# Kernel optimization log

Measured on AMD Instinct MI355X. Metric: run time of the kernel, lower is better.

Reference implementation:

```python
import jax, jax.numpy as jnp
import numpy as np

N = 100000          # nodes
E = 600000          # edges
H = 128             # hidden_dim
CF_DIM = 15         # input_dim - 1
NOISE_DIM = 32
NUM_CLASS = 6       # GraphConstructor.number_of_class
B = 64              # number of graphs in batch
BC = B * NUM_CLASS  # total clusters
LAYER_NUM = 3
NEG_SLOPE = 0.01


def setup_inputs() -> dict:
    key = jax.random.key(0)
    ks = jax.random.split(key, 12)
    cf = jax.random.normal(ks[0], (N, CF_DIM), jnp.float32)
    slf = jax.random.uniform(ks[1], (N,), jnp.float32)
    z = jax.random.normal(ks[2], (N, NOISE_DIM), jnp.float32)
    tr = jax.random.uniform(ks[3], (BC,), jnp.float32)
    W_enc = jax.random.normal(ks[4], (CF_DIM + 1 + NOISE_DIM, H), jnp.float32) * 0.05
    b_enc = jax.random.normal(ks[5], (H,), jnp.float32) * 0.05
    W_m = jax.random.normal(ks[6], (2 * H, H), jnp.float32) * 0.05
    b_m = jax.random.normal(ks[7], (H,), jnp.float32) * 0.05
    W_u = jax.random.normal(ks[8], (3 * H, H), jnp.float32) * 0.05
    b_u = jax.random.normal(ks[9], (H,), jnp.float32) * 0.05
    e = jax.random.randint(ks[10], (2, E), 0, N, jnp.int64)
    cc = jax.random.randint(ks[11], (N,), 0, BC, jnp.int64)
    cfb = cc // NUM_CLASS  # batch index consistent with global cluster index
    return {"cf": cf, "slf": slf, "z": z, "tr": tr,
            "W_enc": W_enc, "b_enc": b_enc, "W_m": W_m, "b_m": b_m,
            "W_u": W_u, "b_u": b_u, "e": e, "cc": cc, "cfb": cfb}


def _segment_mean(x, idx, num_segments):
    s = jax.ops.segment_sum(x, idx, num_segments=num_segments)
    c = jax.ops.segment_sum(jnp.ones((x.shape[0],), x.dtype), idx, num_segments=num_segments)
    return s / jnp.maximum(c, 1.0)[:, None]


def reference(cf, slf, z, tr, W_enc, b_enc, W_m, b_m, W_u, b_u, e, cc, cfb):
    # encoder: x = enc(cat(cf, slf, z))  (Linear, no activation since act='')
    x = jnp.concatenate([cf, slf[:, None], z], axis=-1) @ W_enc + b_enc  # [N, H]
    src, dst = e[0], e[1]  # PyG: x_j = x[src], x_i = x[dst], aggregate at dst
    for _ in range(LAYER_NUM):
        # message: MLP(cat(feature_i, feature_j)) per edge, mean-aggregated at dst
        msg = jnp.concatenate([x[dst], x[src]], axis=-1) @ W_m + b_m  # [E, H]
        aggr = _segment_mean(msg, dst, N)                              # [N, H]
        # cluster avg_pool scaled by target ratio, broadcast back to nodes
        pooled = _segment_mean(x, cc, BC) * tr[:, None]                # [BC, H]
        node_pool = pooled[cc]                                         # [N, H]
        upd = jnp.concatenate([x, aggr, node_pool], axis=-1) @ W_u + b_u
        upd = jnp.where(upd > 0, upd, NEG_SLOPE * upd)                 # LeakyReLU
        x = x + upd                                                    # residual
    return x
```

## Files before the change

### kernel.cpp

```cpp
#include <hip/hip_runtime.h>
#include <hip/hip_bf16.h>

#define N_NODES 100000
#define N_EDGES 600000
#define HD 128
#define NBC 384
#define SCAN_B 98
#define MAXFIX 4096
#define TILES ((N_NODES + 63) / 64)
#define GRID_F 521
#define AGG_B (N_NODES / 4)
#define CAPB 16384

typedef __attribute__((ext_vector_type(8))) short s8v;
typedef __attribute__((ext_vector_type(4))) short s4v;
typedef __attribute__((ext_vector_type(4))) float f4v;
typedef __hip_bfloat16 bf16;

static __device__ __forceinline__ float bf2f(bf16 v) { return __bfloat162float(v); }
static __device__ __forceinline__ bf16 f2bf(float v) { return __float2bfloat16(v); }
static __device__ __forceinline__ float sh2f(short s) { bf16 h = *(bf16*)&s; return bf2f(h); }
static __device__ __forceinline__ short f2sh(float v) { bf16 h = f2bf(v); return *(short*)&h; }
static __device__ __forceinline__ float ldraw(const void* p, int i, int fp32) {
    return fp32 ? ((const float*)p)[i] : bf2f(((const bf16*)p)[i]);
}

static __device__ __forceinline__ void gl2lds16(const void* g, void* l) {
    __builtin_amdgcn_global_load_lds(
        (const __attribute__((address_space(1))) void*)g,
        (__attribute__((address_space(3))) void*)l, 16, 0, 0);
}

__global__ void k_init(const unsigned short* __restrict__ wraw, const int* __restrict__ eraw,
                       int* __restrict__ flags, int* __restrict__ deg,
                       int* __restrict__ ccount, int* __restrict__ n0cnt,
                       int* __restrict__ bcur) {
    int b = blockIdx.x, t = threadIdx.x;
    if (b == 0) {
        if (t < 64) {
            int bad = 0;
            for (int k = 0; k < 16; k++) {
                unsigned int u = ((unsigned int)wraw[t * 16 + k]) << 16;
                float f = fabsf(__uint_as_float(u));
                if (!(f <= 1e4f)) bad = 1;
            }
            unsigned long long m = __ballot(bad);
            if (t == 0) {
                flags[0] = m ? 1 : 0;
                flags[1] = (eraw[1] == 0 && eraw[3] == 0 && eraw[5] == 0 && eraw[7] == 0) ? 1 : 0;
            }
        }
    } else if (b <= 98) {
        int i = (b - 1) * 256 + t;
        if (i < 25000) ((int4*)deg)[i] = make_int4(0, 0, 0, 0);
    } else {
        if (t < 96) ((int4*)ccount)[t] = make_int4(0, 0, 0, 0);
        if (t == 96) *n0cnt = 0;
        if (t >= 128 && t < 128 + SCAN_B) bcur[t - 128] = 0;
    }
}

#define F_EDGE 586
#define F_XIN  (F_EDGE + 391)
#define F_CC   (F_XIN + 391)
#define F_WU   (F_CC + 192)
#define F_WM   (F_WU + 128)
#define F_WET  (F_WM + 32)
#define F_BC   (F_WET + 1)
#define F_TR   (F_BC + 2)
__global__ void k_ffront(const int* __restrict__ flags,
                         const void* cf_r, const void* slf_r, const void* z_r,
                         const void* tr_r, const void* Wenc_r, const void* benc_r,
                         const void* Wm_r, const void* bm_r, const void* Wu_r,
                         const void* bu_r, const int* __restrict__ e_r,
                         const int* __restrict__ cc_r,
                         bf16* __restrict__ xin, bf16* __restrict__ trc,
                         bf16* __restrict__ Wuc, bf16* __restrict__ Wmc,
                         bf16* __restrict__ buc, int* __restrict__ ccc,
                         int* __restrict__ deg, int* __restrict__ ccount,
                         bf16* __restrict__ Wet, float* __restrict__ bc,
                         float* __restrict__ bcenc,
                         int* __restrict__ bcur, int* __restrict__ ebuf) {
    __shared__ short scfs[3840];
    __shared__ int hist[SCAN_B], hbase[SCAN_B], lcur[SCAN_B];
    int b = blockIdx.x, t = threadIdx.x;
    int fp32 = flags[0];
    if (b < F_EDGE) {
        int i64f = flags[1];
        int e0 = b * 1024;
        if (t < SCAN_B) { hist[t] = 0; lcur[t] = 0; }
        __syncthreads();
        int sv[4], dv[4], bk[4];
#pragma unroll
        for (int k = 0; k < 4; k++) {
            int i = e0 + k * 256 + t;
            if (i < N_EDGES) {
                sv[k] = i64f ? e_r[2 * i] : e_r[i];
                dv[k] = i64f ? e_r[2 * (N_EDGES + i)] : e_r[N_EDGES + i];
                bk[k] = dv[k] >> 10;
                atomicAdd(&hist[bk[k]], 1);
                atomicAdd(&deg[dv[k]], 1);
            } else bk[k] = -1;
        }
        __syncthreads();
        if (t < SCAN_B && hist[t] > 0) hbase[t] = atomicAdd(&bcur[t], hist[t]);
        __syncthreads();
#pragma unroll
        for (int k = 0; k < 4; k++) {
            if (bk[k] >= 0) {
                int rel = hbase[bk[k]] + atomicAdd(&lcur[bk[k]], 1);
                if (rel < CAPB) ebuf[bk[k] * CAPB + rel] = (sv[k] << 10) | (dv[k] & 1023);
            }
        }
    } else if (b < F_XIN) {
        int bb = b - F_EDGE;
        int base = bb * 256;
        int cnt = min(3840, 1500000 - base * 15);
        if (fp32) {
            const float* cfp = (const float*)cf_r + (size_t)base * 15;
            f4v c0, c1, c2, c3;
            int e0 = t * 4, e1 = (256 + t) * 4, e2 = (512 + t) * 4, e3 = (768 + t) * 4;
            if (e0 < cnt) c0 = *(const f4v*)(cfp + e0);
            if (e1 < cnt) c1 = *(const f4v*)(cfp + e1);
            if (e2 < cnt) c2 = *(const f4v*)(cfp + e2);
            if (e3 < cnt) c3 = *(const f4v*)(cfp + e3);
            if (e0 < cnt) { for (int j = 0; j < 4; j++) scfs[e0 + j] = f2sh(c0[j]); }
            if (e1 < cnt) { for (int j = 0; j < 4; j++) scfs[e1 + j] = f2sh(c1[j]); }
            if (e2 < cnt) { for (int j = 0; j < 4; j++) scfs[e2 + j] = f2sh(c2[j]); }
            if (e3 < cnt) { for (int j = 0; j < 4; j++) scfs[e3 + j] = f2sh(c3[j]); }
        } else {
            const short* cfp = (const short*)cf_r + (size_t)base * 15;
            s8v c0, c1;
            int e0 = t * 8, e1 = (256 + t) * 8;
            if (e0 < cnt) c0 = *(const s8v*)(cfp + e0);
            if (e1 < cnt) c1 = *(const s8v*)(cfp + e1);
            if (e0 < cnt) *(s8v*)(scfs + e0) = c0;
            if (e1 < cnt) *(s8v*)(scfs + e1) = c1;
        }
        __syncthreads();
        int node = base + t;
        if (node >= N_NODES) return;
        short* xr = (short*)xin + (size_t)node * 64;
        const short* c = scfs + t * 15;
        s8v o0, o1;
#pragma unroll
        for (int r = 0; r < 8; r++) o0[r] = c[r];
#pragma unroll
        for (int r = 0; r < 7; r++) o1[r] = c[8 + r];
        o1[7] = fp32 ? f2sh(((const float*)slf_r)[node]) : ((const short*)slf_r)[node];
        if (fp32) {
            const float* zp = (const float*)z_r + (size_t)node * 32;
            f4v z0 = *(const f4v*)(zp +  0), z1 = *(const f4v*)(zp +  4);
            f4v z2 = *(const f4v*)(zp +  8), z3 = *(const f4v*)(zp + 12);
            f4v z4 = *(const f4v*)(zp + 16), z5 = *(const f4v*)(zp + 20);
            f4v z6 = *(const f4v*)(zp + 24), z7 = *(const f4v*)(zp + 28);
            s8v w0, w1, w2, w3;
#pragma unroll
            for (int r = 0; r < 4; r++) {
                w0[r] = f2sh(z0[r]); w0[4 + r] = f2sh(z1[r]);
                w1[r] = f2sh(z2[r]); w1[4 + r] = f2sh(z3[r]);
                w2[r] = f2sh(z4[r]); w2[4 + r] = f2sh(z5[r]);
                w3[r] = f2sh(z6[r]); w3[4 + r] = f2sh(z7[r]);
            }
            *(s8v*)(xr) = o0; *(s8v*)(xr + 8) = o1;
            *(s8v*)(xr + 16) = w0; *(s8v*)(xr + 24) = w1;
            *(s8v*)(xr + 32) = w2; *(s8v*)(xr + 40) = w3;
        } else {
            const short* zp = (const short*)z_r + (size_t)node * 32;
            s8v w0 = *(const s8v*)(zp), w1 = *(const s8v*)(zp + 8);
            s8v w2 = *(const s8v*)(zp + 16), w3 = *(const s8v*)(zp + 24);
            *(s8v*)(xr) = o0; *(s8v*)(xr + 8) = o1;
            *(s8v*)(xr + 16) = w0; *(s8v*)(xr + 24) = w1;
            *(s8v*)(xr + 32) = w2; *(s8v*)(xr + 40) = w3;
        }
        s8v zz = {0, 0, 0, 0, 0, 0, 0, 0};
        *(s8v*)(xr + 48) = zz;
        *(s8v*)(xr + 56) = zz;
    } else if (b < F_CC) {
        int i64f = flags[1];
        int i = (b - F_XIN) * 256 + t;
        if (i < N_NODES) {
            int v = i64f ? cc_r[2 * i] : cc_r[i];
            ccc[i] = v;
            atomicAdd(&ccount[v], 1);
        }
    } else if (b < F_WU) {
        int i = (b - F_CC) * 256 + t;
        Wuc[i] = f2bf(ldraw(Wu_r, i, fp32));
    } else if (b < F_WM) {
        int i = (b - F_WU) * 256 + t;
        Wmc[i] = f2bf(ldraw(Wm_r, i, fp32));
    } else if (b < F_WET) {
        int i = (b - F_WM) * 256 + t;
        int w = i >> 6, kk = i & 63;
        float v = (kk < 48) ? ldraw(Wenc_r, kk * 128 + w, fp32) : 0.f;
        Wet[i] = f2bf(v);
    } else if (b < F_BC) {
        if (t < 128) {
            float acc = ldraw(bu_r, t, fp32);
            for (int j = 0; j < 128; j++)
                acc += ldraw(bm_r, j, fp32) * ldraw(Wu_r, (128 + j) * 128 + t, fp32);
            bc[t] = acc;
        } else {
            bcenc[t - 128] = ldraw(benc_r, t - 128, fp32);
            buc[t - 128] = f2bf(ldraw(bu_r, t - 128, fp32));
        }
    } else {
        int i = (b - F_BC) * 256 + t;
        if (i < 384) trc[i] = f2bf(ldraw(tr_r, i, fp32));
    }
}

__global__ void k_scan_a2(const int* __restrict__ deg, int* __restrict__ rowptr,
                          int* __restrict__ bsum, const int* __restrict__ ccount,
                          int* __restrict__ coff, int* __restrict__ ccur) {
    __shared__ int sd[1024];
    int t = threadIdx.x;
    if (blockIdx.x < SCAN_B) {
        int i = blockIdx.x * 1024 + t;
        int v = (i < N_NODES) ? deg[i] : 0;
        sd[t] = v;
        __syncthreads();
#pragma unroll
        for (int off = 1; off < 1024; off <<= 1) {
            int u = (t >= off) ? sd[t - off] : 0;
            __syncthreads();
            sd[t] += u;
            __syncthreads();
        }
        if (i < N_NODES) rowptr[i] = sd[t] - v;
        if (t == 1023) bsum[blockIdx.x] = sd[t];
    } else {
        int v = (t < NBC) ? ccount[t] : 0;
        sd[t] = v;
        __syncthreads();
#pragma unroll
        for (int off = 1; off < 1024; off <<= 1) {
            int u = (t >= off) ? sd[t - off] : 0;
            __syncthreads();
            sd[t] += u;
            __syncthreads();
        }
        if (t < NBC) {
            int ex = sd[t] - v;
            coff[t] = ex;
            ccur[t] = ex;
            if (t == NBC - 1) coff[NBC] = sd[t];
        }
    }
}

#define M_SC 98
#define M_W  (M_SC + 6)
#define M_CF (M_W + 98)
#define M_L0 (M_CF + 98)
__global__ void k_mid(int* __restrict__ rowptr, const int* __restrict__ bsum,
                      const bf16* __restrict__ Wmc, const bf16* __restrict__ Wuc,
                      bf16* __restrict__ Wc,
                      const int* __restrict__ ccc, int* __restrict__ ccur,
                      int* __restrict__ cnodes,
                      const int* __restrict__ deg, int* __restrict__ n0list,
                      int* __restrict__ n0cnt) {
    __shared__ short wm[4][2048];
    __shared__ int h[NBC], cb[NBC];
    __shared__ int sb[128];
    __shared__ int offs;
    int b = blockIdx.x, t = threadIdx.x;
    if (b < M_SC) {
        if (t < 128) sb[t] = (t < b) ? bsum[t] : 0;
        __syncthreads();
        if (t == 0) {
            int s = 0;
            for (int k = 0; k < 128; k++) s += sb[k];
            offs = s;
        }
        __syncthreads();
        int i = b * 1024 + t;
        if (i < N_NODES) rowptr[i] = rowptr[i] + offs;
        if (b == 0 && t == 0) rowptr[N_NODES] = N_EDGES;
    } else if (b < M_W) {
        int kw = b - M_SC;
        int sub = t >> 8, lt = t & 255;
        int bp = kw * 4 + sub;
        int w = lt & 127, g = lt >> 7;
        int kk0 = bp * 16 + g * 8;
        if (kk0 >= 256) {
            s8v ov;
#pragma unroll
            for (int n = 0; n < 8; n++)
                ov[n] = *((const short*)Wuc + (kk0 + n) * 128 + w);
            *(s8v*)((short*)Wc + w * 384 + kk0) = ov;
            return;
        }
        *(s8v*)(wm[sub] + lt * 8) = *(const s8v*)((const short*)Wmc + bp * 2048 + lt * 8);
        __syncthreads();
        float acc[8];
#pragma unroll
        for (int n = 0; n < 8; n++) acc[n] = 0.f;
        const short* wup = (const short*)Wuc + 128 * 128 + w;
        const short* wmb = wm[sub] + (g * 8) * 128;
#pragma unroll 4
        for (int j = 0; j < 128; j++) {
            float wu = sh2f(wup[j * 128]);
#pragma unroll
            for (int n = 0; n < 8; n++)
                acc[n] += sh2f(wmb[n * 128 + j]) * wu;
        }
        s8v ov;
#pragma unroll
        for (int n = 0; n < 8; n++) {
            int kk = kk0 + n;
            float base = (kk < 128) ? sh2f(*((const short*)Wuc + kk * 128 + w)) : 0.f;
            ov[n] = f2sh(acc[n] + base);
        }
        *(s8v*)((short*)Wc + w * 384 + kk0) = ov;
    } else if (b < M_CF) {
        int base = (b - M_W) << 10;
        int node = base + t;
        if (t < NBC) h[t] = 0;
        __syncthreads();
        int cls = (node < N_NODES) ? ccc[node] : -1;
        if (cls >= 0) atomicAdd(&h[cls], 1);
        __syncthreads();
        if (t < NBC) {
            cb[t] = h[t] ? atomicAdd(&ccur[t], h[t]) : 0;
            h[t] = 0;
        }
        __syncthreads();
        if (cls >= 0) {
            int p = cb[cls] + atomicAdd(&h[cls], 1);
            cnodes[p] = node;
        }
    } else {
        int i = (b - M_CF) * 1024 + t;
        if (i < N_NODES && deg[i] == 0) {
            int p = atomicAdd(n0cnt, 1);
            if (p < MAXFIX) n0list[p] = i;
        }
    }
}

#define K5_EN 1563
#define K5_PC (K5_EN + SCAN_B)
__global__ void k_front(const bf16* __restrict__ xin, const bf16* __restrict__ Wet,
                        const float* __restrict__ bcenc, bf16* __restrict__ xb,
                        const int* __restrict__ rowptr, const int* __restrict__ ebuf,
                        int* __restrict__ colx) {
    __shared__ int cur[1024];
    int b = blockIdx.x;
    if (b >= K5_EN) {
        int bb = b - K5_EN;
        int base = bb << 10;
        int nlim = min(1024, N_NODES - base);
        for (int i = threadIdx.x; i < nlim; i += 256) cur[i] = rowptr[base + i];
        __syncthreads();
        int cnt = rowptr[base + nlim] - rowptr[base];
        const int* eb = ebuf + bb * CAPB;
        for (int e = threadIdx.x; e < cnt; e += 256) {
            int v = eb[e];
            int p = atomicAdd(&cur[v & 1023], 1);
            colx[p] = v >> 10;
        }
        return;
    }
    int tid = threadIdx.x;
    int r0 = b * 64;
    int wave = tid >> 6, lane = tid & 63, quad = lane >> 4, nidx = lane & 15;
    int colbase = wave * 32;

    int arow[4];
#pragma unroll
    for (int rt = 0; rt < 4; rt++) {
        int gr = r0 + rt * 16 + nidx;
        arow[rt] = (gr < N_NODES) ? gr : (N_NODES - 1);
    }
    f4v acc[4][2];
#pragma unroll
    for (int rt = 0; rt < 4; rt++)
#pragma unroll
        for (int ct = 0; ct < 2; ct++) acc[rt][ct] = (f4v){0.f, 0.f, 0.f, 0.f};

#pragma unroll
    for (int s = 0; s < 2; s++) {
        int k0 = s * 32;
        s8v bfrag[4];
#pragma unroll
        for (int rt = 0; rt < 4; rt++)
            bfrag[rt] = *(const s8v*)((const short*)xin + (size_t)arow[rt] * 64 + k0 + quad * 8);
#pragma unroll
        for (int ct = 0; ct < 2; ct++) {
            s8v wfr = *(const s8v*)((const short*)Wet + (colbase + ct * 16 + nidx) * 64 + k0 + quad * 8);
#pragma unroll
            for (int rt = 0; rt < 4; rt++)
                acc[rt][ct] = __builtin_amdgcn_mfma_f32_16x16x32_bf16(wfr, bfrag[rt], acc[rt][ct], 0, 0, 0);
        }
    }
#pragma unroll
    for (int rt = 0; rt < 4; rt++) {
        int gr = r0 + rt * 16 + nidx;
        if (gr < N_NODES) {
#pragma unroll
            for (int ct = 0; ct < 2; ct++) {
                int wc0 = colbase + ct * 16 + quad * 4;
                f4v bv = *(const f4v*)(bcenc + wc0);
                size_t idx = (size_t)gr * HD + wc0;
                s4v ob;
#pragma unroll
                for (int r = 0; r < 4; r++) ob[r] = f2sh(acc[rt][ct][r] + bv[r]);
                *(s4v*)((short*)xb + idx) = ob;
            }
        }
    }
}

__global__ void k_aggpool(const bf16* __restrict__ xb, const int* __restrict__ rowptr,
                          const int* __restrict__ colx, bf16* __restrict__ mb,
                          const int* __restrict__ coff, const int* __restrict__ cnodes,
                          const bf16* __restrict__ trc, bf16* __restrict__ pooled) {
    __shared__ float red[8][128];
    int tid = threadIdx.x;
    if (blockIdx.x < NBC) {
        int cl = blockIdx.x;
        int lo = coff[cl], hi = coff[cl + 1];
        int cnt = hi - lo;
        int slot = tid >> 5, cg = tid & 31;
        float a0 = 0.f, a1 = 0.f, a2 = 0.f, a3 = 0.f;
        for (int i = lo + slot; i < hi; i += 8) {
            int nd = cnodes[i];
            s4v v = *(const s4v*)((const short*)xb + (size_t)nd * HD + cg * 4);
            a0 += sh2f(v[0]); a1 += sh2f(v[1]); a2 += sh2f(v[2]); a3 += sh2f(v[3]);
        }
        red[slot][cg * 4 + 0] = a0;
        red[slot][cg * 4 + 1] = a1;
        red[slot][cg * 4 + 2] = a2;
        red[slot][cg * 4 + 3] = a3;
        __syncthreads();
        if (tid < 128) {
            float s = 0.f;
#pragma unroll
            for (int k = 0; k < 8; k++) s += red[k][tid];
            float v = s / (float)(cnt > 1 ? cnt : 1) * bf2f(trc[cl]);
            pooled[cl * HD + tid] = f2bf(v);
        }
        return;
    }
    int wave = tid >> 6, lane = tid & 63;
    int node = (blockIdx.x - NBC) * 4 + wave;
    if (node >= N_NODES) return;
    int half = lane >> 5;
    int l = lane & 31;
    int lo = rowptr[node], hi = rowptr[node + 1];
    float a0 = 0.f, a1 = 0.f, a2 = 0.f, a3 = 0.f;
    for (int j0 = lo + half; j0 < hi; j0 += 8) {
        int i1 = j0 + 2, i2 = j0 + 4, i3 = j0 + 6;
        int s0 = colx[j0];
        int s1 = colx[i1 < hi ? i1 : j0];
        int s2 = colx[i2 < hi ? i2 : j0];
        int s3 = colx[i3 < hi ? i3 : j0];
        float m1 = (i1 < hi) ? 1.f : 0.f;
        float m2 = (i2 < hi) ? 1.f : 0.f;
        float m3 = (i3 < hi) ? 1.f : 0.f;
        s4v v0 = *(const s4v*)((const short*)xb + (size_t)s0 * HD + l * 4);
        s4v v1 = *(const s4v*)((const short*)xb + (size_t)s1 * HD + l * 4);
        s4v v2 = *(const s4v*)((const short*)xb + (size_t)s2 * HD + l * 4);
        s4v v3 = *(const s4v*)((const short*)xb + (size_t)s3 * HD + l * 4);
        a0 += sh2f(v0[0]) + m1 * sh2f(v1[0]) + m2 * sh2f(v2[0]) + m3 * sh2f(v3[0]);
        a1 += sh2f(v0[1]) + m1 * sh2f(v1[1]) + m2 * sh2f(v2[1]) + m3 * sh2f(v3[1]);
        a2 += sh2f(v0[2]) + m1 * sh2f(v1[2]) + m2 * sh2f(v2[2]) + m3 * sh2f(v3[2]);
        a3 += sh2f(v0[3]) + m1 * sh2f(v1[3]) + m2 * sh2f(v2[3]) + m3 * sh2f(v3[3]);
    }
    a0 += __shfl_down(a0, 32);
    a1 += __shfl_down(a1, 32);
    a2 += __shfl_down(a2, 32);
    a3 += __shfl_down(a3, 32);
    if (half == 0) {
        int d = hi - lo;
        float inv = 1.0f / (float)(d > 1 ? d : 1);
        s4v o;
        o[0] = f2sh(a0 * inv); o[1] = f2sh(a1 * inv);
        o[2] = f2sh(a2 * inv); o[3] = f2sh(a3 * inv);
        *(s4v*)((short*)mb + (size_t)node * HD + l * 4) = o;
    }
}

__global__ __launch_bounds__(256, 2) void k_fused2(
    const bf16* __restrict__ xb, const bf16* __restrict__ mb, const bf16* __restrict__ pooled,
    const bf16* __restrict__ Wc, const float* __restrict__ bc,
    const int* __restrict__ cc, const int* __restrict__ deg,
    const bf16* __restrict__ Wuc, const bf16* __restrict__ buc,
    const int* __restrict__ n0list, const int* __restrict__ n0cnt,
    bf16* __restrict__ xbo, const int* __restrict__ flags,
    void* __restrict__ out, int last) {
    __shared__ short Lx[64 * 128];
    __shared__ short Lm[64 * 128];
    __shared__ short Lp[64 * 128];
    __shared__ float fxv[128];
    __shared__ float fpv[128];
    int tid = threadIdx.x;
    int wave = tid >> 6, lane = tid & 63, quad = lane >> 4, nidx = lane & 15;
    int colbase = wave * 32;
    int fp32out = flags[0];

    s8v wfr[12][2];
#pragma unroll
    for (int ct = 0; ct < 2; ct++) {
        int wcol = colbase + ((nidx >> 2) << 3) + ct * 4 + (nidx & 3);
        const short* wrow = (const short*)Wc + (size_t)wcol * 384 + quad * 8;
#pragma unroll
        for (int s = 0; s < 12; s++) wfr[s][ct] = *(const s8v*)(wrow + s * 32);
    }
    int cb2 = colbase + quad * 8;
    f4v bv0 = *(const f4v*)(bc + cb2);
    f4v bv1 = *(const f4v*)(bc + cb2 + 4);

    int srow = lane >> 4;
    int sc = lane & 15;

    for (int t = blockIdx.x; t < TILES; t += GRID_F) {
        int r0 = t * 64;
#pragma unroll
        for (int ii = 0; ii < 4; ii++) {
            int i = wave * 4 + ii;
            int lr = i * 4 + srow;
            int gr = r0 + lr;
            int grc = (gr < N_NODES) ? gr : (N_NODES - 1);
            int gc = sc ^ (lr & 15);
            gl2lds16((const short*)xb + (size_t)grc * HD + gc * 8, (char*)Lx + i * 1024);
            gl2lds16((const short*)mb + (size_t)grc * HD + gc * 8, (char*)Lm + i * 1024);
            int ci = cc[grc];
            gl2lds16((const short*)pooled + (size_t)ci * HD + gc * 8, (char*)Lp + i * 1024);
        }
        __syncthreads();

        f4v acc[4][2];
#pragma unroll
        for (int rt = 0; rt < 4; rt++)
#pragma unroll
            for (int ct = 0; ct < 2; ct++) acc[rt][ct] = (f4v){0.f, 0.f, 0.f, 0.f};

#pragma unroll
        for (int s = 0; s < 12; s++) {
            const short* Ls = (s < 4) ? Lx : ((s < 8) ? Lm : Lp);
            int c = (s & 3) * 4 + quad;
            s8v bfrag[4];
#pragma unroll
            for (int rt = 0; rt < 4; rt++) {
                int row = rt * 16 + nidx;
                int slot = c ^ nidx;
                bfrag[rt] = *(const s8v*)(Ls + row * 128 + slot * 8);
            }
#pragma unroll
            for (int ct = 0; ct < 2; ct++)
#pragma unroll
                for (int rt = 0; rt < 4; rt++)
                    acc[rt][ct] = __builtin_amdgcn_mfma_f32_16x16x32_bf16(wfr[s][ct], bfrag[rt], acc[rt][ct], 0, 0, 0);
        }

#pragma unroll
        for (int rt = 0; rt < 4; rt++) {
            int gr = r0 + rt * 16 + nidx;
            if (gr < N_NODES && deg[gr] > 0) {
                int row = rt * 16 + nidx;
                int slot = ((colbase >> 3) + quad) ^ nidx;
                s8v xo = *(const s8v*)(Lx + row * 128 + slot * 8);
                size_t idx = (size_t)gr * HD + cb2;
                float nv[8];
#pragma unroll
                for (int r = 0; r < 4; r++) {
                    float v0 = acc[rt][0][r] + bv0[r];
                    v0 = (v0 > 0.f) ? v0 : 0.01f * v0;
                    nv[r] = sh2f(xo[r]) + v0;
                    float v1 = acc[rt][1][r] + bv1[r];
                    v1 = (v1 > 0.f) ? v1 : 0.01f * v1;
                    nv[4 + r] = sh2f(xo[4 + r]) + v1;
                }
                if (last) {
                    if (fp32out) {
                        f4v o0 = {nv[0], nv[1], nv[2], nv[3]};
                        f4v o1 = {nv[4], nv[5], nv[6], nv[7]};
                        *(f4v*)((float*)out + idx) = o0;
                        *(f4v*)((float*)out + idx + 4) = o1;
                    } else {
                        s8v ob;
#pragma unroll
                        for (int r = 0; r < 8; r++) ob[r] = f2sh(nv[r]);
                        *(s8v*)((short*)out + idx) = ob;
                    }
                } else {
                    s8v ob;
#pragma unroll
                    for (int r = 0; r < 8; r++) ob[r] = f2sh(nv[r]);
                    *(s8v*)((short*)xbo + idx) = ob;
                }
            }
        }
        __syncthreads();
    }

    int cnt0 = *n0cnt;
    if (cnt0 > MAXFIX) cnt0 = MAXFIX;
    for (int j = blockIdx.x; j < cnt0; j += gridDim.x) {
        int v = n0list[j];
        if (tid < 128) {
            fxv[tid] = bf2f(xb[(size_t)v * HD + tid]);
            fpv[tid] = bf2f(pooled[cc[v] * HD + tid]);
        }
        __syncthreads();
        if (tid < 128) {
            float acc = bf2f(buc[tid]);
            for (int k = 0; k < 128; k++)
                acc += fxv[k] * bf2f(Wuc[k * 128 + tid]) + fpv[k] * bf2f(Wuc[(256 + k) * 128 + tid]);
            float u = acc > 0.f ? acc : 0.01f * acc;
            size_t idx = (size_t)v * HD + tid;
            float nv = fxv[tid] + u;
            if (last) {
                if (fp32out) ((float*)out)[idx] = nv;
                else ((bf16*)out)[idx] = f2bf(nv);
            } else {
                xbo[idx] = f2bf(nv);
            }
        }
        __syncthreads();
    }
}

extern "C" void kernel_launch(void* const* d_in, const int* in_sizes, int n_in,
                              void* d_out, int out_size, void* d_ws, size_t ws_size,
                              hipStream_t stream) {
    const void* cf_r = d_in[0];
    const void* slf_r = d_in[1];
    const void* z_r = d_in[2];
    const void* tr_r = d_in[3];
    const void* Wenc_r = d_in[4];
    const void* benc_r = d_in[5];
    const void* Wm_r = d_in[6];
    const void* bm_r = d_in[7];
    const void* Wu_r = d_in[8];
    const void* bu_r = d_in[9];
    const int* e_r = (const int*)d_in[10];
    const int* cc_r = (const int*)d_in[11];

    char* w = (char*)d_ws;
    auto alloc = [&](size_t bytes) -> char* {
        char* p = w;
        w += (bytes + 63) & ~(size_t)63;
        return p;
    };
    bf16* xb0 = (bf16*)alloc((size_t)N_NODES * HD * 2);
    bf16* xb1 = (bf16*)alloc((size_t)N_NODES * HD * 2);
    bf16* mb = (bf16*)alloc((size_t)N_NODES * HD * 2);
    bf16* xin = (bf16*)alloc((size_t)N_NODES * 64 * 2);
    bf16* Wc = (bf16*)alloc(128 * 384 * 2);
    float* bc = (float*)alloc(128 * 4);
    bf16* Wet = (bf16*)alloc(128 * 64 * 2);
    float* bcenc = (float*)alloc(128 * 4);
    bf16* pooled = (bf16*)alloc(NBC * HD * 2);
    int* deg = (int*)alloc(N_NODES * 4);
    int* rowptr = (int*)alloc((N_NODES + 1) * 4);
    int* colx = (int*)alloc(N_EDGES * 4);
    int* ccount = (int*)alloc(NBC * 4);
    int* coff = (int*)alloc((NBC + 1) * 4);
    int* ccur = (int*)alloc(NBC * 4);
    int* cnodes = (int*)alloc(N_NODES * 4);
    int* flags = (int*)alloc(64);
    int* bsum = (int*)alloc(SCAN_B * 4);
    int* n0list = (int*)alloc(MAXFIX * 4);
    int* n0cnt = (int*)alloc(64);
    bf16* trc = (bf16*)alloc(384 * 2);
    bf16* Wuc = (bf16*)alloc(49152 * 2);
    bf16* Wmc = (bf16*)alloc(32768 * 2);
    bf16* buc = (bf16*)alloc(128 * 2);
    int* ccc = (int*)alloc(N_NODES * 4);
    int* bcur = (int*)alloc(SCAN_B * 4);
    int* ebuf = (int*)alloc((size_t)SCAN_B * CAPB * 4);

    k_init<<<100, 256, 0, stream>>>((const unsigned short*)Wenc_r, e_r, flags,
                                    deg, ccount, n0cnt, bcur);
    k_ffront<<<F_TR, 256, 0, stream>>>(flags, cf_r, slf_r, z_r, tr_r, Wenc_r, benc_r,
                                       Wm_r, bm_r, Wu_r, bu_r, e_r, cc_r,
                                       xin, trc, Wuc, Wmc, buc, ccc, deg, ccount,
                                       Wet, bc, bcenc, bcur, ebuf);
    k_scan_a2<<<SCAN_B + 1, 1024, 0, stream>>>(deg, rowptr, bsum, ccount, coff, ccur);
    k_mid<<<M_L0, 1024, 0, stream>>>(rowptr, bsum, Wmc, Wuc, Wc,
                                     ccc, ccur, cnodes, deg, n0list, n0cnt);
    k_front<<<K5_PC, 256, 0, stream>>>(xin, Wet, bcenc, xb0, rowptr, ebuf, colx);

    bf16* xbufs[2] = {xb0, xb1};
    for (int layer = 0; layer < 3; layer++) {
        bf16* xbi = xbufs[layer & 1];
        bf16* xbo = xbufs[(layer + 1) & 1];
        int last = (layer == 2);
        k_aggpool<<<AGG_B + NBC, 256, 0, stream>>>(xbi, rowptr, colx, mb,
                                                   coff, cnodes, trc, pooled);
        k_fused2<<<GRID_F, 256, 0, stream>>>(xbi, mb, pooled, Wc, bc, ccc, deg,
                                             Wuc, buc, n0list, n0cnt,
                                             xbo, flags, d_out, last);
    }
}
```

Baseline: 446.1 us.

## Build CSR from destination buckets instead of global degree atomics and scan

The CSR build no longer uses per-edge global degree atomics and a 100K-element two-pass scan. Per-bucket degree histograms are now computed in LDS inside k_mid, with a small scan over bucket totals, and rowptr, deg, the zero-degree list and colx are all filled in that same block. Cluster counting now uses a per-block LDS histogram before the global atomics, and the old deg-zeroing blocks in k_init are removed. Together these cut global atomics and kernel work in the preprocessing phase. The cost is that each bucket is now handled by a single 1024-thread block doing serial LDS atomics.

```diff
diff --git a/kernel.cpp b/kernel.cpp
--- a/kernel.cpp
+++ b/kernel.cpp
@@ -32,9 +32,8 @@
 }
 
 __global__ void k_init(const unsigned short* __restrict__ wraw, const int* __restrict__ eraw,
-                       int* __restrict__ flags, int* __restrict__ deg,
-                       int* __restrict__ ccount, int* __restrict__ n0cnt,
-                       int* __restrict__ bcur) {
+                       int* __restrict__ flags, int* __restrict__ ccount,
+                       int* __restrict__ n0cnt, int* __restrict__ bcur) {
     int b = blockIdx.x, t = threadIdx.x;
     if (b == 0) {
         if (t < 64) {
@@ -50,9 +49,6 @@
                 flags[1] = (eraw[1] == 0 && eraw[3] == 0 && eraw[5] == 0 && eraw[7] == 0) ? 1 : 0;
             }
         }
-    } else if (b <= 98) {
-        int i = (b - 1) * 256 + t;
-        if (i < 25000) ((int4*)deg)[i] = make_int4(0, 0, 0, 0);
     } else {
         if (t < 96) ((int4*)ccount)[t] = make_int4(0, 0, 0, 0);
         if (t == 96) *n0cnt = 0;
@@ -62,7 +58,7 @@
 
 #define F_EDGE 586
 #define F_XIN  (F_EDGE + 391)
-#define F_CC   (F_XIN + 391)
+#define F_CC   (F_XIN + 98)
 #define F_WU   (F_CC + 192)
 #define F_WM   (F_WU + 128)
 #define F_WET  (F_WM + 32)
@@ -77,12 +73,13 @@
                          bf16* __restrict__ xin, bf16* __restrict__ trc,
                          bf16* __restrict__ Wuc, bf16* __restrict__ Wmc,
                          bf16* __restrict__ buc, int* __restrict__ ccc,
-                         int* __restrict__ deg, int* __restrict__ ccount,
+                         int* __restrict__ ccount,
                          bf16* __restrict__ Wet, float* __restrict__ bc,
                          float* __restrict__ bcenc,
                          int* __restrict__ bcur, int* __restrict__ ebuf) {
     __shared__ short scfs[3840];
     __shared__ int hist[SCAN_B], hbase[SCAN_B], lcur[SCAN_B];
+    __shared__ int ch[NBC];
     int b = blockIdx.x, t = threadIdx.x;
     int fp32 = flags[0];
     if (b < F_EDGE) {
@@ -99,7 +96,6 @@
                 dv[k] = i64f ? e_r[2 * (N_EDGES + i)] : e_r[N_EDGES + i];
                 bk[k] = dv[k] >> 10;
                 atomicAdd(&hist[bk[k]], 1);
-                atomicAdd(&deg[dv[k]], 1);
             } else bk[k] = -1;
         }
         __syncthreads();
@@ -178,11 +174,24 @@
         *(s8v*)(xr + 56) = zz;
     } else if (b < F_CC) {
         int i64f = flags[1];
-        int i = (b - F_XIN) * 256 + t;
-        if (i < N_NODES) {
-            int v = i64f ? cc_r[2 * i] : cc_r[i];
-            ccc[i] = v;
-            atomicAdd(&ccount[v], 1);
+        int nbase = (b - F_XIN) << 10;
+        int nlim = min(1024, N_NODES - nbase);
+        for (int j = t; j < NBC; j += 256) ch[j] = 0;
+        __syncthreads();
+#pragma unroll
+        for (int k = 0; k < 4; k++) {
+            int li = k * 256 + t;
+            if (li < nlim) {
+                int i = nbase + li;
+                int v = i64f ? cc_r[2 * i] : cc_r[i];
+                ccc[i] = v;
+                atomicAdd(&ch[v], 1);
+            }
+        }
+        __syncthreads();
+        for (int j = t; j < NBC; j += 256) {
+            int c = ch[j];
+            if (c) atomicAdd(&ccount[j], c);
         }
     } else if (b < F_WU) {
         int i = (b - F_CC) * 256 + t;
@@ -198,6 +207,7 @@
     } else if (b < F_BC) {
         if (t < 128) {
             float acc = ldraw(bu_r, t, fp32);
+#pragma unroll 4
             for (int j = 0; j < 128; j++)
                 acc += ldraw(bm_r, j, fp32) * ldraw(Wu_r, (128 + j) * 128 + t, fp32);
             bc[t] = acc;
@@ -211,31 +221,30 @@
     }
 }
 
-__global__ void k_scan_a2(const int* __restrict__ deg, int* __restrict__ rowptr,
-                          int* __restrict__ bsum, const int* __restrict__ ccount,
-                          int* __restrict__ coff, int* __restrict__ ccur) {
+__global__ void k_scan2(const int* __restrict__ bcur, int* __restrict__ bbase,
+                        const int* __restrict__ ccount, int* __restrict__ coff,
+                        int* __restrict__ ccur, int* __restrict__ rowptr) {
     __shared__ int sd[1024];
     int t = threadIdx.x;
-    if (blockIdx.x < SCAN_B) {
-        int i = blockIdx.x * 1024 + t;
-        int v = (i < N_NODES) ? deg[i] : 0;
+    if (blockIdx.x == 0) {
+        int v = (t < SCAN_B) ? bcur[t] : 0;
         sd[t] = v;
         __syncthreads();
 #pragma unroll
-        for (int off = 1; off < 1024; off <<= 1) {
+        for (int off = 1; off < 128; off <<= 1) {
             int u = (t >= off) ? sd[t - off] : 0;
             __syncthreads();
             sd[t] += u;
             __syncthreads();
         }
-        if (i < N_NODES) rowptr[i] = sd[t] - v;
-        if (t == 1023) bsum[blockIdx.x] = sd[t];
+        if (t < SCAN_B) bbase[t] = sd[t] - v;
+        if (t == 0) rowptr[N_NODES] = N_EDGES;
     } else {
         int v = (t < NBC) ? ccount[t] : 0;
         sd[t] = v;
         __syncthreads();
 #pragma unroll
-        for (int off = 1; off < 1024; off <<= 1) {
+        for (int off = 1; off < 512; off <<= 1) {
             int u = (t >= off) ? sd[t - off] : 0;
             __syncthreads();
             sd[t] += u;
@@ -250,36 +259,24 @@
     }
 }
 
-#define M_SC 98
-#define M_W  (M_SC + 6)
-#define M_CF (M_W + 98)
-#define M_L0 (M_CF + 98)
-__global__ void k_mid(int* __restrict__ rowptr, const int* __restrict__ bsum,
-                      const bf16* __restrict__ Wmc, const bf16* __restrict__ Wuc,
+#define M_W  6
+#define M_PC (M_W + SCAN_B)
+#define M_CF (M_PC + SCAN_B)
+__global__ void k_mid(const bf16* __restrict__ Wmc, const bf16* __restrict__ Wuc,
                       bf16* __restrict__ Wc,
                       const int* __restrict__ ccc, int* __restrict__ ccur,
                       int* __restrict__ cnodes,
-                      const int* __restrict__ deg, int* __restrict__ n0list,
-                      int* __restrict__ n0cnt) {
+                      const int* __restrict__ bcur, const int* __restrict__ bbase,
+                      const int* __restrict__ ebuf,
+                      int* __restrict__ rowptr, int* __restrict__ deg,
+                      int* __restrict__ colx,
+                      int* __restrict__ n0list, int* __restrict__ n0cnt) {
     __shared__ short wm[4][2048];
+    __shared__ int h2[1024], sd[1024];
     __shared__ int h[NBC], cb[NBC];
-    __shared__ int sb[128];
-    __shared__ int offs;
     int b = blockIdx.x, t = threadIdx.x;
-    if (b < M_SC) {
-        if (t < 128) sb[t] = (t < b) ? bsum[t] : 0;
-        __syncthreads();
-        if (t == 0) {
-            int s = 0;
-            for (int k = 0; k < 128; k++) s += sb[k];
-            offs = s;
-        }
-        __syncthreads();
-        int i = b * 1024 + t;
-        if (i < N_NODES) rowptr[i] = rowptr[i] + offs;
-        if (b == 0 && t == 0) rowptr[N_NODES] = N_EDGES;
-    } else if (b < M_W) {
-        int kw = b - M_SC;
+    if (b < M_W) {
+        int kw = b;
         int sub = t >> 8, lt = t & 255;
         int bp = kw * 4 + sub;
         int w = lt & 127, g = lt >> 7;
@@ -314,8 +311,46 @@
             ov[n] = f2sh(acc[n] + base);
         }
         *(s8v*)((short*)Wc + w * 384 + kk0) = ov;
-    } else if (b < M_CF) {
-        int base = (b - M_W) << 10;
+    } else if (b < M_PC) {
+        int bb = b - M_W;
+        int nbase = bb << 10;
+        int nlim = min(1024, N_NODES - nbase);
+        int cnt = min(bcur[bb], CAPB);
+        int base = bbase[bb];
+        h2[t] = 0;
+        __syncthreads();
+        const int* eb = ebuf + bb * CAPB;
+        for (int e = t; e < cnt; e += 1024) atomicAdd(&h2[eb[e] & 1023], 1);
+        __syncthreads();
+        int myDeg = h2[t];
+        sd[t] = myDeg;
+        __syncthreads();
+#pragma unroll
+        for (int off = 1; off < 1024; off <<= 1) {
+            int u = (t >= off) ? sd[t - off] : 0;
+            __syncthreads();
+            sd[t] += u;
+            __syncthreads();
+        }
+        int ex = sd[t] - myDeg;
+        if (t < nlim) {
+            rowptr[nbase + t] = base + ex;
+            deg[nbase + t] = myDeg;
+            if (myDeg == 0) {
+                int p = atomicAdd(n0cnt, 1);
+                if (p < MAXFIX) n0list[p] = nbase + t;
+            }
+        }
+        __syncthreads();
+        h2[t] = ex;
+        __syncthreads();
+        for (int e = t; e < cnt; e += 1024) {
+            int v = eb[e];
+            int p = atomicAdd(&h2[v & 1023], 1);
+            colx[base + p] = v >> 10;
+        }
+    } else {
+        int base = (b - M_PC) << 10;
         int node = base + t;
         if (t < NBC) h[t] = 0;
         __syncthreads();
@@ -331,40 +366,13 @@
             int p = cb[cls] + atomicAdd(&h[cls], 1);
             cnodes[p] = node;
         }
-    } else {
-        int i = (b - M_CF) * 1024 + t;
-        if (i < N_NODES && deg[i] == 0) {
-            int p = atomicAdd(n0cnt, 1);
-            if (p < MAXFIX) n0list[p] = i;
-        }
-    }
-}
-
-#define K5_EN 1563
-#define K5_PC (K5_EN + SCAN_B)
+    }
+}
+
 __global__ void k_front(const bf16* __restrict__ xin, const bf16* __restrict__ Wet,
-                        const float* __restrict__ bcenc, bf16* __restrict__ xb,
-                        const int* __restrict__ rowptr, const int* __restrict__ ebuf,
-                        int* __restrict__ colx) {
-    __shared__ int cur[1024];
-    int b = blockIdx.x;
-    if (b >= K5_EN) {
-        int bb = b - K5_EN;
-        int base = bb << 10;
-        int nlim = min(1024, N_NODES - base);
-        for (int i = threadIdx.x; i < nlim; i += 256) cur[i] = rowptr[base + i];
-        __syncthreads();
-        int cnt = rowptr[base + nlim] - rowptr[base];
-        const int* eb = ebuf + bb * CAPB;
-        for (int e = threadIdx.x; e < cnt; e += 256) {
-            int v = eb[e];
-            int p = atomicAdd(&cur[v & 1023], 1);
-            colx[p] = v >> 10;
-        }
-        return;
-    }
+                        const float* __restrict__ bcenc, bf16* __restrict__ xb) {
     int tid = threadIdx.x;
-    int r0 = b * 64;
+    int r0 = blockIdx.x * 64;
     int wave = tid >> 6, lane = tid & 63, quad = lane >> 4, nidx = lane & 15;
     int colbase = wave * 32;
 
@@ -663,7 +671,6 @@
     int* ccur = (int*)alloc(NBC * 4);
     int* cnodes = (int*)alloc(N_NODES * 4);
     int* flags = (int*)alloc(64);
-    int* bsum = (int*)alloc(SCAN_B * 4);
     int* n0list = (int*)alloc(MAXFIX * 4);
     int* n0cnt = (int*)alloc(64);
     bf16* trc = (bf16*)alloc(384 * 2);
@@ -672,18 +679,20 @@
     bf16* buc = (bf16*)alloc(128 * 2);
     int* ccc = (int*)alloc(N_NODES * 4);
     int* bcur = (int*)alloc(SCAN_B * 4);
+    int* bbase = (int*)alloc(SCAN_B * 4);
     int* ebuf = (int*)alloc((size_t)SCAN_B * CAPB * 4);
 
-    k_init<<<100, 256, 0, stream>>>((const unsigned short*)Wenc_r, e_r, flags,
-                                    deg, ccount, n0cnt, bcur);
+    k_init<<<2, 256, 0, stream>>>((const unsigned short*)Wenc_r, e_r, flags,
+                                  ccount, n0cnt, bcur);
     k_ffront<<<F_TR, 256, 0, stream>>>(flags, cf_r, slf_r, z_r, tr_r, Wenc_r, benc_r,
                                        Wm_r, bm_r, Wu_r, bu_r, e_r, cc_r,
-                                       xin, trc, Wuc, Wmc, buc, ccc, deg, ccount,
+                                       xin, trc, Wuc, Wmc, buc, ccc, ccount,
                                        Wet, bc, bcenc, bcur, ebuf);
-    k_scan_a2<<<SCAN_B + 1, 1024, 0, stream>>>(deg, rowptr, bsum, ccount, coff, ccur);
-    k_mid<<<M_L0, 1024, 0, stream>>>(rowptr, bsum, Wmc, Wuc, Wc,
-                                     ccc, ccur, cnodes, deg, n0list, n0cnt);
-    k_front<<<K5_PC, 256, 0, stream>>>(xin, Wet, bcenc, xb0, rowptr, ebuf, colx);
+    k_scan2<<<2, 1024, 0, stream>>>(bcur, bbase, ccount, coff, ccur, rowptr);
+    k_mid<<<M_CF, 1024, 0, stream>>>(Wmc, Wuc, Wc, ccc, ccur, cnodes,
+                                     bcur, bbase, ebuf, rowptr, deg, colx,
+                                     n0list, n0cnt);
+    k_front<<<TILES, 256, 0, stream>>>(xin, Wet, bcenc, xb0);
 
     bf16* xbufs[2] = {xb0, xb1};
     for (int layer = 0; layer < 3; layer++) {
```

Measured after the change: 386.8 us. 13.3% less time.
